# Performance work log

Measured on AMD Instinct MI355X. Metric: run time of the kernel, lower is better.

The kernel has to match this reference:

```python
import jax, jax.numpy as jnp
import numpy as np

INPUT_DIM, HIDDEN, HEADS = 310, 64, 8
WINDOW, PERIOD = 5, 3
NEG_INF = -jnp.inf


def _masks(seq_len):
    i = jnp.arange(seq_len)[:, None]
    j = jnp.arange(seq_len)[None, :]
    local = jnp.abs(i - j) <= WINDOW
    sparse = (j % PERIOD == 0) | (i == j)
    to_add = lambda m: jnp.where(m, 0.0, NEG_INF).astype(jnp.float32)
    return to_add(local), to_add(sparse)


def _mha(xp, in_w, in_b, out_w, out_b, mask):
    # xp: [B,S,E]; in_w: [3E,E]; out_w: [E,E]; mask: [S,S] additive
    B, S, E = xp.shape
    d = E // HEADS
    qkv = xp @ in_w.T + in_b                      # [B,S,3E]
    q, k, v = jnp.split(qkv, 3, axis=-1)
    split_heads = lambda t: t.reshape(B, S, HEADS, d).transpose(0, 2, 1, 3)
    q, k, v = split_heads(q), split_heads(k), split_heads(v)
    scores = jnp.einsum('bhqd,bhkd->bhqk', q, k) / jnp.sqrt(jnp.float32(d))
    scores = scores + mask                         # broadcast [S,S]
    attn = jax.nn.softmax(scores, axis=-1)
    o = jnp.einsum('bhqk,bhkd->bhqd', attn, v)
    o = o.transpose(0, 2, 1, 3).reshape(B, S, E)
    return o @ out_w.T + out_b


def setup_inputs() -> dict:
    key = jax.random.key(0)
    ks = jax.random.split(key, 16)
    E = HIDDEN
    s = lambda fan: 1.0 / np.sqrt(fan)
    u = lambda k, shape, fan: jax.random.uniform(k, shape, jnp.float32, -s(fan), s(fan))
    return {
        'x': jax.random.normal(ks[0], (16, 1024, INPUT_DIM), jnp.float32),
        'proj_w': u(ks[1], (E, INPUT_DIM), INPUT_DIM),
        'proj_b': u(ks[2], (E,), INPUT_DIM),
        'loc_in_w': u(ks[3], (3 * E, E), E),
        'loc_in_b': jnp.zeros((3 * E,), jnp.float32),
        'loc_out_w': u(ks[4], (E, E), E),
        'loc_out_b': jnp.zeros((E,), jnp.float32),
        'glob_in_w': u(ks[5], (3 * E, E), E),
        'glob_in_b': jnp.zeros((3 * E,), jnp.float32),
        'glob_out_w': u(ks[6], (E, E), E),
        'glob_out_b': jnp.zeros((E,), jnp.float32),
        'fusion_w': u(ks[7], (E, 2 * E), 2 * E),
        'fusion_b': u(ks[8], (E,), 2 * E),
        'pool_w1': u(ks[9], (E // 2, E), E),
        'pool_b1': u(ks[10], (E // 2,), E),
        'pool_w2': u(ks[11], (1, E // 2), E // 2),
        'pool_b2': u(ks[12], (1,), E // 2),
    }


def reference(x, proj_w, proj_b, loc_in_w, loc_in_b, loc_out_w, loc_out_b,
              glob_in_w, glob_in_b, glob_out_w, glob_out_b,
              fusion_w, fusion_b, pool_w1, pool_b1, pool_w2, pool_b2):
    B, S, _ = x.shape
    local_mask, sparse_mask = _masks(S)
    xp = x @ proj_w.T + proj_b                     # [B,S,E]
    local_out = _mha(xp, loc_in_w, loc_in_b, loc_out_w, loc_out_b, local_mask)
    global_out = _mha(xp, glob_in_w, glob_in_b, glob_out_w, glob_out_b, sparse_mask)
    fused = jnp.concatenate([local_out, global_out], axis=-1) @ fusion_w.T + fusion_b
    scores = jnp.tanh(fused @ pool_w1.T + pool_b1) @ pool_w2.T + pool_b2  # [B,S,1]
    w = jax.nn.softmax(scores, axis=1)             # softmax over seq dim
    return jnp.sum(fused * w, axis=1)              # [B,E]
```

## Files before the change

### kernel.cpp

```cpp
#include <hip/hip_runtime.h>


typedef __attribute__((ext_vector_type(8))) short short8;
typedef __attribute__((ext_vector_type(4))) float float4v;

#define INV_SQRT8 0.3535533905932738f

__device__ __forceinline__ float4 ld4(const float* p) { return *(const float4*)p; }

__device__ __forceinline__ float4 f4fma(float s, float4 w, float4 a) {
  a.x = fmaf(s, w.x, a.x); a.y = fmaf(s, w.y, a.y);
  a.z = fmaf(s, w.z, a.z); a.w = fmaf(s, w.w, a.w);
  return a;
}

__device__ __forceinline__ void bsplit(float x, short& h, short& l) {
  unsigned xb = __float_as_uint(x);
  unsigned hb = (xb + 0x7fffu + ((xb >> 16) & 1u)) & 0xffff0000u;
  h = (short)(hb >> 16);
  float lf = x - __uint_as_float(hb);
  unsigned lb = __float_as_uint(lf);
  l = (short)((lb + 0x7fffu + ((lb >> 16) & 1u)) >> 16);
}

__global__ __launch_bounds__(256) void prep_w(
    const float* __restrict__ pw, const float* __restrict__ liw,
    const float* __restrict__ giw, const float* __restrict__ fw,
    const float* __restrict__ low, const float* __restrict__ gow,
    const float* __restrict__ lob, const float* __restrict__ gob,
    const float* __restrict__ fb,
    short* __restrict__ wb, float* __restrict__ bc, float* __restrict__ numden)
{
  unsigned idx = blockIdx.x * 256 + threadIdx.x;
  float v; unsigned ho, lo_;
  if (idx < 20480u) {
    unsigned r = idx / 320u, k = idx - r * 320u;
    v = (k < 310u) ? pw[r * 310u + k] : 0.f;
    ho = 0u + idx; lo_ = 20480u + idx;
  } else if (idx < 32768u) {
    unsigned i = idx - 20480u; v = liw[i]; ho = 40960u + i; lo_ = 53248u + i;
  } else if (idx < 45056u) {
    unsigned i = idx - 32768u; v = giw[i]; ho = 65536u + i; lo_ = 77824u + i;
  } else {
    unsigned i = idx - 45056u;
    unsigned n = i >> 7, k = i & 127u;
    float s = 0.f;
    if (k < 64u) {
      for (int e = 0; e < 64; e++) s += fw[n * 128 + e] * low[e * 64 + k];
    } else {
      for (int e = 0; e < 64; e++) s += fw[n * 128 + 64 + e] * gow[e * 64 + (k - 64u)];
    }
    v = s; ho = 90112u + i; lo_ = 98304u + i;
  }
  short h, l; bsplit(v, h, l);
  wb[ho] = h; wb[lo_] = l;
  if (idx < 64u) {
    float b = fb[idx];
    for (int e = 0; e < 64; e++)
      b += lob[e] * fw[idx * 128 + e] + gob[e] * fw[idx * 128 + 64 + e];
    bc[idx] = b;
  }
  if (idx < 1040u) numden[idx] = 0.f;
}

__global__ __launch_bounds__(256) void gemm_proj(
    const float* __restrict__ X,
    const short* __restrict__ Wh, const short* __restrict__ Wl,
    const float* __restrict__ bias,
    short* __restrict__ Ch, short* __restrict__ Cl)
{
  const int lane = threadIdx.x & 63;
  const int w = threadIdx.x >> 6;
  const int q = lane >> 4, r = lane & 15;
  const int m0 = blockIdx.x * 64 + w * 16;
  const int n0 = blockIdx.y * 32;

  float bv0 = bias[n0 + r], bv1 = bias[n0 + 16 + r];
  float4v acc0 = {bv0, bv0, bv0, bv0};
  float4v acc1 = {bv1, bv1, bv1, bv1};

  const float* arow = X + (size_t)(m0 + r) * 310;

  #pragma unroll
  for (int ks = 0; ks < 10; ks++) {
    const int k0 = ks * 32 + q * 8;
    float av[8];
    if (ks < 9) {
      const float* ap = arow + k0;
      #pragma unroll
      for (int t = 0; t < 4; t++) {
        float2 f = *(const float2*)(ap + t * 2);
        av[t*2] = f.x; av[t*2+1] = f.y;
      }
    } else {
      #pragma unroll
      for (int j = 0; j < 8; j++) {
        int kidx = k0 + j;
        av[j] = (kidx < 310) ? arow[kidx] : 0.f;
      }
    }
    short8 ah, al;
    #pragma unroll
    for (int i = 0; i < 8; i++) { short h, l; bsplit(av[i], h, l); ah[i]=h; al[i]=l; }
    short8 bh0 = *(const short8*)(Wh + (size_t)(n0 + r) * 320 + k0);
    short8 bl0 = *(const short8*)(Wl + (size_t)(n0 + r) * 320 + k0);
    short8 bh1 = *(const short8*)(Wh + (size_t)(n0 + 16 + r) * 320 + k0);
    short8 bl1 = *(const short8*)(Wl + (size_t)(n0 + 16 + r) * 320 + k0);
    acc0 = __builtin_amdgcn_mfma_f32_16x16x32_bf16(al, bh0, acc0, 0, 0, 0);
    acc0 = __builtin_amdgcn_mfma_f32_16x16x32_bf16(ah, bl0, acc0, 0, 0, 0);
    acc0 = __builtin_amdgcn_mfma_f32_16x16x32_bf16(ah, bh0, acc0, 0, 0, 0);
    acc1 = __builtin_amdgcn_mfma_f32_16x16x32_bf16(al, bh1, acc1, 0, 0, 0);
    acc1 = __builtin_amdgcn_mfma_f32_16x16x32_bf16(ah, bl1, acc1, 0, 0, 0);
    acc1 = __builtin_amdgcn_mfma_f32_16x16x32_bf16(ah, bh1, acc1, 0, 0, 0);
  }

  #pragma unroll
  for (int e = 0; e < 4; e++) {
    const int row = m0 + q * 4 + e;
    short h, l;
    bsplit(acc0[e], h, l);
    Ch[(size_t)row * 64 + n0 + r] = h; Cl[(size_t)row * 64 + n0 + r] = l;
    bsplit(acc1[e], h, l);
    Ch[(size_t)row * 64 + n0 + 16 + r] = h; Cl[(size_t)row * 64 + n0 + 16 + r] = l;
  }
}

template<int KP>
__global__ __launch_bounds__(256) void gemm_mfma(
    const short* __restrict__ Ah, const short* __restrict__ Al,
    const short* __restrict__ Wh0, const short* __restrict__ Wl0,
    const short* __restrict__ Wh1, const short* __restrict__ Wl1,
    const float* __restrict__ bias0, const float* __restrict__ bias1,
    float* __restrict__ C0, float* __restrict__ C1, int ldc)
{
  const int z = blockIdx.z;
  const short* Wh = z ? Wh1 : Wh0;
  const short* Wl = z ? Wl1 : Wl0;
  const float* bias = z ? bias1 : bias0;
  float* C = z ? C1 : C0;

  const int lane = threadIdx.x & 63;
  const int w = threadIdx.x >> 6;
  const int q = lane >> 4, r = lane & 15;
  const int m0 = blockIdx.x * 64 + w * 16;
  const int n0 = blockIdx.y * 32;

  float bv0 = bias[n0 + r], bv1 = bias[n0 + 16 + r];
  float4v acc0 = {bv0, bv0, bv0, bv0};
  float4v acc1 = {bv1, bv1, bv1, bv1};

  #pragma unroll
  for (int ks = 0; ks < KP / 32; ks++) {
    const int k0 = ks * 32 + q * 8;
    short8 ah = *(const short8*)(Ah + (size_t)(m0 + r) * KP + k0);
    short8 al = *(const short8*)(Al + (size_t)(m0 + r) * KP + k0);
    short8 bh0 = *(const short8*)(Wh + (size_t)(n0 + r) * KP + k0);
    short8 bl0 = *(const short8*)(Wl + (size_t)(n0 + r) * KP + k0);
    short8 bh1 = *(const short8*)(Wh + (size_t)(n0 + 16 + r) * KP + k0);
    short8 bl1 = *(const short8*)(Wl + (size_t)(n0 + 16 + r) * KP + k0);
    acc0 = __builtin_amdgcn_mfma_f32_16x16x32_bf16(al, bh0, acc0, 0, 0, 0);
    acc0 = __builtin_amdgcn_mfma_f32_16x16x32_bf16(ah, bl0, acc0, 0, 0, 0);
    acc0 = __builtin_amdgcn_mfma_f32_16x16x32_bf16(ah, bh0, acc0, 0, 0, 0);
    acc1 = __builtin_amdgcn_mfma_f32_16x16x32_bf16(al, bh1, acc1, 0, 0, 0);
    acc1 = __builtin_amdgcn_mfma_f32_16x16x32_bf16(ah, bl1, acc1, 0, 0, 0);
    acc1 = __builtin_amdgcn_mfma_f32_16x16x32_bf16(ah, bh1, acc1, 0, 0, 0);
  }

  #pragma unroll
  for (int e = 0; e < 4; e++) {
    const int row = m0 + q * 4 + e;
    C[(size_t)row * ldc + n0 + r] = acc0[e];
    C[(size_t)row * ldc + n0 + 16 + r] = acc1[e];
  }
}

__global__ __launch_bounds__(256) void prep_kv_local(
    const float* __restrict__ qkv_g, const float* __restrict__ qkv_l,
    short* __restrict__ KH, short* __restrict__ KL,
    short* __restrict__ VTh, short* __restrict__ VTl,
    float* __restrict__ o_l)
{
  const int u = blockIdx.x;
  if (u < 4224) {
    unsigned idx = (unsigned)u * 256u + threadIdx.x;
    if (idx < 360448u) {
      unsigned bh = idx / 2816u;
      unsigned rem = idx - bh * 2816u;
      unsigned kk = rem >> 3, d = rem & 7u;
      float v = (kk < 342u)
        ? qkv_g[((size_t)((bh >> 3) * 1024 + kk * 3)) * 192 + 64 + (bh & 7u) * 8 + d]
        : 0.f;
      short h, l; bsplit(v, h, l);
      KH[idx] = h; KL[idx] = l;
    } else if (idx < 1081344u) {
      unsigned j = idx - 360448u;
      unsigned bh = j / 5632u;
      unsigned rem = j - bh * 5632u;
      unsigned n = rem / 352u, kk = rem - n * 352u;
      float v;
      if (n < 8u) {
        v = (kk < 342u)
          ? qkv_g[((size_t)((bh >> 3) * 1024 + kk * 3)) * 192 + 128 + (bh & 7u) * 8 + n]
          : 0.f;
      } else {
        v = (n == 8u) ? 1.f : 0.f;
      }
      short h, l; bsplit(v, h, l);
      VTh[j] = h; VTl[j] = l;
    }
  } else {
    int t = (u - 4224) * 256 + threadIdx.x;
    int h = t & 7;
    int i = (t >> 3) & 1023;
    int b = t >> 13;
    const float* base = qkv_l + (size_t)b * 1024 * 192;
    const float* qp = base + (size_t)i * 192 + h * 8;
    float4 q0 = ld4(qp), q1 = ld4(qp + 4);
    float l = 0.f;
    float4 o0 = make_float4(0.f, 0.f, 0.f, 0.f);
    float4 o1 = make_float4(0.f, 0.f, 0.f, 0.f);
    int jlo = i - 5; if (jlo < 0) jlo = 0;
    int jhi = i + 5; if (jhi > 1023) jhi = 1023;
    for (int j = jlo; j <= jhi; j++) {
      const float* kp = base + (size_t)j * 192 + 64 + h * 8;
      float4 k0 = ld4(kp), k1 = ld4(kp + 4);
      float s = q0.x * k0.x + q0.y * k0.y + q0.z * k0.z + q0.w * k0.w
              + q1.x * k1.x + q1.y * k1.y + q1.z * k1.z + q1.w * k1.w;
      float p = __expf(s * INV_SQRT8);
      l += p;
      float4 v0 = ld4(kp + 64), v1 = ld4(kp + 68);
      o0 = f4fma(p, v0, o0);
      o1 = f4fma(p, v1, o1);
    }
    float inv = 1.f / l;
    float* op = o_l + (size_t)(b * 1024 + i) * 64 + h * 8;
    float4 r0, r1;
    r0.x = o0.x * inv; r0.y = o0.y * inv; r0.z = o0.z * inv; r0.w = o0.w * inv;
    r1.x = o1.x * inv; r1.y = o1.y * inv; r1.z = o1.z * inv; r1.w = o1.w * inv;
    *(float4*)op = r0;
    *(float4*)(op + 4) = r1;
  }
}

__global__ __launch_bounds__(256) void mfma_gattn(
    const float* __restrict__ qkv,
    const short* __restrict__ KH, const short* __restrict__ KL,
    const short* __restrict__ VTh, const short* __restrict__ VTl,
    float* __restrict__ o_g, float* __restrict__ pl)
{
  __shared__ short Pbuf[4][2][2][16][32];
  const int b = blockIdx.x, h = blockIdx.y, qt = blockIdx.z;
  const int w = threadIdx.x >> 6, lane = threadIdx.x & 63;
  const int quad = lane >> 4, r = lane & 15;
  const int bh = b * 8 + h;
  const int m0 = qt * 64 + w * 16;

  const short8 z8 = {0,0,0,0,0,0,0,0};
  short8 qh = z8, ql = z8;
  if (quad == 0) {
    const float* qp = qkv + (size_t)(b * 1024 + m0 + r) * 192 + h * 8;
    #pragma unroll
    for (int d = 0; d < 8; d++) { short hh, ll; bsplit(qp[d], hh, ll); qh[d]=hh; ql[d]=ll; }
  }
  const short* kbase  = KH + (size_t)bh * 2816;
  const short* klbase = KL + (size_t)bh * 2816;
  const short* vhbase = VTh + ((size_t)bh * 16 + r) * 352;
  const short* vlbase = VTl + ((size_t)bh * 16 + r) * 352;

  float4v oacc = {0.f, 0.f, 0.f, 0.f};

  for (int kc = 0; kc < 11; kc++) {
    short8 kh0 = z8, kl0 = z8, kh1 = z8, kl1 = z8;
    if (quad == 0) {
      kh0 = *(const short8*)(kbase  + (size_t)(kc * 32 + r) * 8);
      kl0 = *(const short8*)(klbase + (size_t)(kc * 32 + r) * 8);
      kh1 = *(const short8*)(kbase  + (size_t)(kc * 32 + 16 + r) * 8);
      kl1 = *(const short8*)(klbase + (size_t)(kc * 32 + 16 + r) * 8);
    }
    float4v s0 = {0.f,0.f,0.f,0.f}, s1 = {0.f,0.f,0.f,0.f};
    s0 = __builtin_amdgcn_mfma_f32_16x16x32_bf16(qh, kl0, s0, 0, 0, 0);
    s0 = __builtin_amdgcn_mfma_f32_16x16x32_bf16(ql, kh0, s0, 0, 0, 0);
    s0 = __builtin_amdgcn_mfma_f32_16x16x32_bf16(qh, kh0, s0, 0, 0, 0);
    s1 = __builtin_amdgcn_mfma_f32_16x16x32_bf16(qh, kl1, s1, 0, 0, 0);
    s1 = __builtin_amdgcn_mfma_f32_16x16x32_bf16(ql, kh1, s1, 0, 0, 0);
    s1 = __builtin_amdgcn_mfma_f32_16x16x32_bf16(qh, kh1, s1, 0, 0, 0);

    const int par = kc & 1;
    const int key0 = kc * 32 + r, key1 = key0 + 16;
    #pragma unroll
    for (int e = 0; e < 4; e++) {
      float p0 = (key0 < 342) ? __expf(s0[e] * INV_SQRT8) : 0.f;
      float p1 = (key1 < 342) ? __expf(s1[e] * INV_SQRT8) : 0.f;
      short h0, l0, h1, l1; bsplit(p0, h0, l0); bsplit(p1, h1, l1);
      const int qloc = quad * 4 + e;
      Pbuf[w][par][0][qloc][r]      = h0;
      Pbuf[w][par][0][qloc][16 + r] = h1;
      Pbuf[w][par][1][qloc][r]      = l0;
      Pbuf[w][par][1][qloc][16 + r] = l1;
    }
    short8 pA = *(const short8*)&Pbuf[w][par][0][r][quad * 8];
    short8 pB = *(const short8*)&Pbuf[w][par][1][r][quad * 8];
    short8 vh = *(const short8*)(vhbase + kc * 32 + quad * 8);
    short8 vl = *(const short8*)(vlbase + kc * 32 + quad * 8);
    oacc = __builtin_amdgcn_mfma_f32_16x16x32_bf16(pA, vl, oacc, 0, 0, 0);
    oacc = __builtin_amdgcn_mfma_f32_16x16x32_bf16(pB, vh, oacc, 0, 0, 0);
    oacc = __builtin_amdgcn_mfma_f32_16x16x32_bf16(pA, vh, oacc, 0, 0, 0);
  }

  #pragma unroll
  for (int e = 0; e < 4; e++) {
    const int orow = b * 1024 + m0 + quad * 4 + e;
    if (r < 8)       o_g[(size_t)orow * 64 + h * 8 + r] = oacc[e];
    else if (r == 8) pl[(size_t)orow * 8 + h] = oacc[e];
  }
}

__global__ __launch_bounds__(256) void gemm_fuse_score(
    const float* __restrict__ o_l, const float* __restrict__ o_g,
    const float* __restrict__ pl, const float* __restrict__ qkv_g,
    const short* __restrict__ Wh, const short* __restrict__ Wl,
    const float* __restrict__ bc,
    const float* __restrict__ pw1, const float* __restrict__ pb1,
    const float* __restrict__ pw2, const float* __restrict__ pb2,
    float* __restrict__ num, float* __restrict__ den)
{
  __shared__ float Ls[64][68];
  __shared__ float partial[4][64];
  const int tid = threadIdx.x;
  const int lane = tid & 63, w = tid >> 6;
  const int quad = lane >> 4, r = lane & 15;
  const int bx = blockIdx.x;
  const int m0 = bx * 64 + w * 16;

  float4v acc[4];
  #pragma unroll
  for (int g = 0; g < 4; g++) {
    float bv = bc[g * 16 + r];
    float4v t = {bv, bv, bv, bv};
    acc[g] = t;
  }

  #pragma unroll
  for (int ks = 0; ks < 4; ks++) {
    const int k0 = ks * 32 + quad * 8;
    const int row = m0 + r;
    float av[8];
    if (ks < 2) {
      const float* ap = o_l + (size_t)row * 64 + k0;
      float4 f0 = ld4(ap), f1 = ld4(ap + 4);
      av[0]=f0.x; av[1]=f0.y; av[2]=f0.z; av[3]=f0.w;
      av[4]=f1.x; av[5]=f1.y; av[6]=f1.z; av[7]=f1.w;
    } else {
      const int off = k0 - 64;
      const int h = off >> 3;
      const float* op = o_g + (size_t)row * 64 + off;
      float4 O0 = ld4(op), O1 = ld4(op + 4);
      float l = pl[(size_t)row * 8 + h];
      const int i = row & 1023;
      if (i % 3 != 0) {
        const float* base = qkv_g + (size_t)row * 192;
        const float* qp = base + h * 8;
        const float* kpp = base + 64 + h * 8;
        const float* vp = base + 128 + h * 8;
        float4 q0 = ld4(qp), q1 = ld4(qp + 4);
        float4 k0v = ld4(kpp), k1v = ld4(kpp + 4);
        float s = q0.x*k0v.x + q0.y*k0v.y + q0.z*k0v.z + q0.w*k0v.w
                + q1.x*k1v.x + q1.y*k1v.y + q1.z*k1v.z + q1.w*k1v.w;
        float p = __expf(s * INV_SQRT8);
        float4 v0 = ld4(vp), v1 = ld4(vp + 4);
        O0 = f4fma(p, v0, O0); O1 = f4fma(p, v1, O1);
        l += p;
      }
      float inv = 1.f / l;
      av[0]=O0.x*inv; av[1]=O0.y*inv; av[2]=O0.z*inv; av[3]=O0.w*inv;
      av[4]=O1.x*inv; av[5]=O1.y*inv; av[6]=O1.z*inv; av[7]=O1.w*inv;
    }
    short8 ah, al;
    #pragma unroll
    for (int i2 = 0; i2 < 8; i2++) { short h2, l2; bsplit(av[i2], h2, l2); ah[i2]=h2; al[i2]=l2; }
    #pragma unroll
    for (int g = 0; g < 4; g++) {
      short8 bh = *(const short8*)(Wh + (size_t)(g * 16 + r) * 128 + k0);
      short8 bl = *(const short8*)(Wl + (size_t)(g * 16 + r) * 128 + k0);
      acc[g] = __builtin_amdgcn_mfma_f32_16x16x32_bf16(al, bh, acc[g], 0, 0, 0);
      acc[g] = __builtin_amdgcn_mfma_f32_16x16x32_bf16(ah, bl, acc[g], 0, 0, 0);
      acc[g] = __builtin_amdgcn_mfma_f32_16x16x32_bf16(ah, bh, acc[g], 0, 0, 0);
    }
  }

  #pragma unroll
  for (int g = 0; g < 4; g++)
    #pragma unroll
    for (int e = 0; e < 4; e++)
      Ls[w * 16 + quad * 4 + e][g * 16 + r] = acc[g][e];
  __syncthreads();

  float4 fr[16];
  #pragma unroll
  for (int e = 0; e < 16; e++) fr[e] = *(float4*)&Ls[lane][e * 4];

  float psc = 0.f;
  #pragma unroll
  for (int jj = 0; jj < 8; jj++) {
    const int j = w * 8 + jj;
    const float* wr = pw1 + j * 64;
    float hj = pb1[j];
    #pragma unroll
    for (int e = 0; e < 16; e++) {
      float4 wv = ld4(wr + e * 4);
      hj += fr[e].x * wv.x + fr[e].y * wv.y + fr[e].z * wv.z + fr[e].w * wv.w;
    }
    float e2 = __expf(2.f * hj);
    psc += ((e2 - 1.f) / (e2 + 1.f)) * pw2[j];
  }
  partial[w][lane] = psc;
  __syncthreads();
  if (w == 0) {
    const int b = bx >> 4;
    float sc = pb2[0] + partial[0][lane] + partial[1][lane]
             + partial[2][lane] + partial[3][lane];
    float p = __expf(sc);
    #pragma unroll
    for (int e = 0; e < 16; e++) {
      Ls[lane][e*4+0] = p * fr[e].x; Ls[lane][e*4+1] = p * fr[e].y;
      Ls[lane][e*4+2] = p * fr[e].z; Ls[lane][e*4+3] = p * fr[e].w;
    }
    float colsum = 0.f;
    #pragma unroll 8
    for (int s = 0; s < 64; s++) colsum += Ls[s][lane];
    atomicAdd(&num[b * 64 + lane], colsum);
    float ps = p;
    #pragma unroll
    for (int off = 32; off > 0; off >>= 1)
      ps += __shfl_xor(ps, off, 64);
    if (lane == 0) atomicAdd(&den[b], ps);
  }
}

__global__ __launch_bounds__(1024) void finalize(
    const float* __restrict__ num, const float* __restrict__ den,
    float* __restrict__ out)
{
  int t = threadIdx.x;
  out[t] = num[t] / den[t >> 6];
}

extern "C" void kernel_launch(void* const* d_in, const int* in_sizes, int n_in,
                              void* d_out, int out_size, void* d_ws, size_t ws_size,
                              hipStream_t stream)
{
  const float* x          = (const float*)d_in[0];
  const float* proj_w     = (const float*)d_in[1];
  const float* proj_b     = (const float*)d_in[2];
  const float* loc_in_w   = (const float*)d_in[3];
  const float* loc_in_b   = (const float*)d_in[4];
  const float* loc_out_w  = (const float*)d_in[5];
  const float* loc_out_b  = (const float*)d_in[6];
  const float* glob_in_w  = (const float*)d_in[7];
  const float* glob_in_b  = (const float*)d_in[8];
  const float* glob_out_w = (const float*)d_in[9];
  const float* glob_out_b = (const float*)d_in[10];
  const float* fusion_w   = (const float*)d_in[11];
  const float* fusion_b   = (const float*)d_in[12];
  const float* pw1        = (const float*)d_in[13];
  const float* pb1        = (const float*)d_in[14];
  const float* pw2        = (const float*)d_in[15];
  const float* pb2        = (const float*)d_in[16];

  float* ws = (float*)d_ws;
  float* qkv_g = ws;
  short* xph   = (short*)(ws + 3538944);
  short* xpl   = (short*)(ws + 4063232);
  float* qkv_l = ws + 4587520;
  float* o_l   = ws + 7733248;
  float* o_g   = ws + 8781824;
  float* pl    = ws + 9830400;
  short* KH    = (short*)(ws + 9961472);
  short* KL    = (short*)(ws + 10141696);
  short* VTh   = (short*)(ws + 10321920);
  short* VTl   = (short*)(ws + 10682368);
  float* bc    = ws + 11042816;
  float* numden= ws + 11042880;
  float* num   = numden;
  float* den   = numden + 1024;
  short* wb    = (short*)(ws + 11043920);
  short* projh = wb;           short* projl = wb + 20480;
  short* linh  = wb + 40960;   short* linl  = wb + 53248;
  short* ginh  = wb + 65536;   short* ginl  = wb + 77824;
  short* wfh   = wb + 90112;   short* wfl   = wb + 98304;
  float* out   = (float*)d_out;

  dim3 blk(256);
  prep_w<<<208, blk, 0, stream>>>(proj_w, loc_in_w, glob_in_w, fusion_w,
                                  loc_out_w, glob_out_w, loc_out_b, glob_out_b,
                                  fusion_b, wb, bc, numden);
  gemm_proj<<<dim3(256, 2), blk, 0, stream>>>(x, projh, projl, proj_b, xph, xpl);
  gemm_mfma<64><<<dim3(256, 6, 2), blk, 0, stream>>>(
      xph, xpl, linh, linl, ginh, ginl, loc_in_b, glob_in_b,
      qkv_l, qkv_g, 192);
  prep_kv_local<<<4736, blk, 0, stream>>>(qkv_g, qkv_l, KH, KL, VTh, VTl, o_l);
  mfma_gattn<<<dim3(16, 8, 16), blk, 0, stream>>>(qkv_g, KH, KL, VTh, VTl, o_g, pl);
  gemm_fuse_score<<<256, blk, 0, stream>>>(
      o_l, o_g, pl, qkv_g, wfh, wfl, bc, pw1, pb1, pw2, pb2, num, den);
  finalize<<<1, dim3(1024), 0, stream>>>(num, den, out);
}
```

Measured before the change: 191.2 us.

## Fuse projection with QKV GEMM and K/V packing; merge global and local attention

The input projection and both QKV projections now run in one kernel. The projected activations stay in shared memory as bf16 hi/lo pairs instead of going through a global round trip. The same kernel scatters the strided global K and transposed V directly into their packed buffers. The constant padding and ones-row of V is initialised in prep_w, and the global attention and local attention kernels merge into one launch. Together this removes two kernel launches and the xp/qkv re-read passes, at the cost of heavy per-thread register use (24 accumulators) and a grid of only 256 blocks for the fused GEMM.

```diff
diff --git a/kernel.cpp b/kernel.cpp
--- a/kernel.cpp
+++ b/kernel.cpp
@@ -29,58 +29,91 @@
     const float* __restrict__ low, const float* __restrict__ gow,
     const float* __restrict__ lob, const float* __restrict__ gob,
     const float* __restrict__ fb,
-    short* __restrict__ wb, float* __restrict__ bc, float* __restrict__ numden)
+    short* __restrict__ wb, float* __restrict__ bc, float* __restrict__ numden,
+    short* __restrict__ VTh, short* __restrict__ VTl)
 {
   unsigned idx = blockIdx.x * 256 + threadIdx.x;
-  float v; unsigned ho, lo_;
-  if (idx < 20480u) {
-    unsigned r = idx / 320u, k = idx - r * 320u;
-    v = (k < 310u) ? pw[r * 310u + k] : 0.f;
-    ho = 0u + idx; lo_ = 20480u + idx;
-  } else if (idx < 32768u) {
-    unsigned i = idx - 20480u; v = liw[i]; ho = 40960u + i; lo_ = 53248u + i;
-  } else if (idx < 45056u) {
-    unsigned i = idx - 32768u; v = giw[i]; ho = 65536u + i; lo_ = 77824u + i;
+  if (idx < 53248u) {
+    float v; unsigned ho, lo_;
+    if (idx < 20480u) {
+      unsigned r = idx / 320u, k = idx - r * 320u;
+      v = (k < 310u) ? pw[r * 310u + k] : 0.f;
+      ho = 0u + idx; lo_ = 20480u + idx;
+    } else if (idx < 32768u) {
+      unsigned i = idx - 20480u; v = liw[i]; ho = 40960u + i; lo_ = 53248u + i;
+    } else if (idx < 45056u) {
+      unsigned i = idx - 32768u; v = giw[i]; ho = 65536u + i; lo_ = 77824u + i;
+    } else {
+      unsigned i = idx - 45056u;
+      unsigned n = i >> 7, k = i & 127u;
+      float s = 0.f;
+      if (k < 64u) {
+        for (int e = 0; e < 64; e++) s += fw[n * 128 + e] * low[e * 64 + k];
+      } else {
+        for (int e = 0; e < 64; e++) s += fw[n * 128 + 64 + e] * gow[e * 64 + (k - 64u)];
+      }
+      v = s; ho = 90112u + i; lo_ = 98304u + i;
+    }
+    short h, l; bsplit(v, h, l);
+    wb[ho] = h; wb[lo_] = l;
+    if (idx < 64u) {
+      float b = fb[idx];
+      for (int e = 0; e < 64; e++)
+        b += lob[e] * fw[idx * 128 + e] + gob[e] * fw[idx * 128 + 64 + e];
+      bc[idx] = b;
+    }
+    if (idx < 1040u) numden[idx] = 0.f;
   } else {
-    unsigned i = idx - 45056u;
-    unsigned n = i >> 7, k = i & 127u;
-    float s = 0.f;
-    if (k < 64u) {
-      for (int e = 0; e < 64; e++) s += fw[n * 128 + e] * low[e * 64 + k];
-    } else {
-      for (int e = 0; e < 64; e++) s += fw[n * 128 + 64 + e] * gow[e * 64 + (k - 64u)];
-    }
-    v = s; ho = 90112u + i; lo_ = 98304u + i;
-  }
-  short h, l; bsplit(v, h, l);
-  wb[ho] = h; wb[lo_] = l;
-  if (idx < 64u) {
-    float b = fb[idx];
-    for (int e = 0; e < 64; e++)
-      b += lob[e] * fw[idx * 128 + e] + gob[e] * fw[idx * 128 + 64 + e];
-    bc[idx] = b;
-  }
-  if (idx < 1040u) numden[idx] = 0.f;
-}
-
-__global__ __launch_bounds__(256) void gemm_proj(
+    unsigned t = idx - 53248u;
+    if (t < 370688u) {
+      unsigned pos; short hv = 0;
+      if (t < 360448u) {
+        unsigned bh = t / 2816u;
+        unsigned rem = t - bh * 2816u;
+        unsigned n8 = rem / 352u;
+        unsigned kk = rem - n8 * 352u;
+        pos = (bh * 16u + 8u + n8) * 352u + kk;
+        if (n8 == 0u) hv = (short)0x3F80;
+      } else {
+        unsigned t2 = t - 360448u;
+        unsigned bh = t2 / 80u;
+        unsigned rem = t2 - bh * 80u;
+        unsigned n = rem / 10u;
+        unsigned kk = 342u + (rem - n * 10u);
+        pos = (bh * 16u + n) * 352u + kk;
+      }
+      VTh[pos] = hv; VTl[pos] = 0;
+    }
+  }
+}
+
+__global__ __launch_bounds__(256) void gemm_proj_qkv(
     const float* __restrict__ X,
-    const short* __restrict__ Wh, const short* __restrict__ Wl,
-    const float* __restrict__ bias,
-    short* __restrict__ Ch, short* __restrict__ Cl)
+    const short* __restrict__ PWh, const short* __restrict__ PWl,
+    const float* __restrict__ pb,
+    const short* __restrict__ LWh, const short* __restrict__ LWl,
+    const short* __restrict__ GWh, const short* __restrict__ GWl,
+    const float* __restrict__ lb, const float* __restrict__ gb,
+    float* __restrict__ qkv_l, float* __restrict__ qkv_g,
+    short* __restrict__ KH, short* __restrict__ KL,
+    short* __restrict__ VTh, short* __restrict__ VTl)
 {
+  __shared__ __align__(16) short XPH[64][72];
+  __shared__ __align__(16) short XPL[64][72];
   const int lane = threadIdx.x & 63;
   const int w = threadIdx.x >> 6;
   const int q = lane >> 4, r = lane & 15;
-  const int m0 = blockIdx.x * 64 + w * 16;
-  const int n0 = blockIdx.y * 32;
-
-  float bv0 = bias[n0 + r], bv1 = bias[n0 + 16 + r];
-  float4v acc0 = {bv0, bv0, bv0, bv0};
-  float4v acc1 = {bv1, bv1, bv1, bv1};
-
+  const int mloc = w * 16;
+  const int m0 = blockIdx.x * 64 + mloc;
+
+  float4v accp[4];
+  #pragma unroll
+  for (int g = 0; g < 4; g++) {
+    float bv = pb[g * 16 + r];
+    float4v t = {bv, bv, bv, bv};
+    accp[g] = t;
+  }
   const float* arow = X + (size_t)(m0 + r) * 310;
-
   #pragma unroll
   for (int ks = 0; ks < 10; ks++) {
     const int k0 = ks * 32 + q * 8;
@@ -102,114 +135,161 @@
     short8 ah, al;
     #pragma unroll
     for (int i = 0; i < 8; i++) { short h, l; bsplit(av[i], h, l); ah[i]=h; al[i]=l; }
-    short8 bh0 = *(const short8*)(Wh + (size_t)(n0 + r) * 320 + k0);
-    short8 bl0 = *(const short8*)(Wl + (size_t)(n0 + r) * 320 + k0);
-    short8 bh1 = *(const short8*)(Wh + (size_t)(n0 + 16 + r) * 320 + k0);
-    short8 bl1 = *(const short8*)(Wl + (size_t)(n0 + 16 + r) * 320 + k0);
-    acc0 = __builtin_amdgcn_mfma_f32_16x16x32_bf16(al, bh0, acc0, 0, 0, 0);
-    acc0 = __builtin_amdgcn_mfma_f32_16x16x32_bf16(ah, bl0, acc0, 0, 0, 0);
-    acc0 = __builtin_amdgcn_mfma_f32_16x16x32_bf16(ah, bh0, acc0, 0, 0, 0);
-    acc1 = __builtin_amdgcn_mfma_f32_16x16x32_bf16(al, bh1, acc1, 0, 0, 0);
-    acc1 = __builtin_amdgcn_mfma_f32_16x16x32_bf16(ah, bl1, acc1, 0, 0, 0);
-    acc1 = __builtin_amdgcn_mfma_f32_16x16x32_bf16(ah, bh1, acc1, 0, 0, 0);
-  }
-
+    #pragma unroll
+    for (int g = 0; g < 4; g++) {
+      short8 bh = *(const short8*)(PWh + (size_t)(g * 16 + r) * 320 + k0);
+      short8 bl = *(const short8*)(PWl + (size_t)(g * 16 + r) * 320 + k0);
+      accp[g] = __builtin_amdgcn_mfma_f32_16x16x32_bf16(al, bh, accp[g], 0, 0, 0);
+      accp[g] = __builtin_amdgcn_mfma_f32_16x16x32_bf16(ah, bl, accp[g], 0, 0, 0);
+      accp[g] = __builtin_amdgcn_mfma_f32_16x16x32_bf16(ah, bh, accp[g], 0, 0, 0);
+    }
+  }
+  #pragma unroll
+  for (int g = 0; g < 4; g++)
+    #pragma unroll
+    for (int e = 0; e < 4; e++) {
+      short h, l; bsplit(accp[g][e], h, l);
+      XPH[mloc + q * 4 + e][g * 16 + r] = h;
+      XPL[mloc + q * 4 + e][g * 16 + r] = l;
+    }
+
+  float4v acc[2][12];
+  #pragma unroll
+  for (int nf = 0; nf < 12; nf++) {
+    float bv0 = lb[nf * 16 + r], bv1 = gb[nf * 16 + r];
+    float4v t0 = {bv0, bv0, bv0, bv0};
+    float4v t1 = {bv1, bv1, bv1, bv1};
+    acc[0][nf] = t0; acc[1][nf] = t1;
+  }
+  #pragma unroll
+  for (int ks = 0; ks < 2; ks++) {
+    const int k0 = ks * 32 + q * 8;
+    short8 ah = *(const short8*)&XPH[mloc + r][k0];
+    short8 al = *(const short8*)&XPL[mloc + r][k0];
+    #pragma unroll
+    for (int nf = 0; nf < 12; nf++) {
+      short8 bh0 = *(const short8*)(LWh + (size_t)(nf * 16 + r) * 64 + k0);
+      short8 bl0 = *(const short8*)(LWl + (size_t)(nf * 16 + r) * 64 + k0);
+      acc[0][nf] = __builtin_amdgcn_mfma_f32_16x16x32_bf16(al, bh0, acc[0][nf], 0, 0, 0);
+      acc[0][nf] = __builtin_amdgcn_mfma_f32_16x16x32_bf16(ah, bl0, acc[0][nf], 0, 0, 0);
+      acc[0][nf] = __builtin_amdgcn_mfma_f32_16x16x32_bf16(ah, bh0, acc[0][nf], 0, 0, 0);
+      short8 bh1 = *(const short8*)(GWh + (size_t)(nf * 16 + r) * 64 + k0);
+      short8 bl1 = *(const short8*)(GWl + (size_t)(nf * 16 + r) * 64 + k0);
+      acc[1][nf] = __builtin_amdgcn_mfma_f32_16x16x32_bf16(al, bh1, acc[1][nf], 0, 0, 0);
+      acc[1][nf] = __builtin_amdgcn_mfma_f32_16x16x32_bf16(ah, bl1, acc[1][nf], 0, 0, 0);
+      acc[1][nf] = __builtin_amdgcn_mfma_f32_16x16x32_bf16(ah, bh1, acc[1][nf], 0, 0, 0);
+    }
+  }
+
+  const int b = m0 >> 10;
+  const int bh8 = b * 8;
   #pragma unroll
   for (int e = 0; e < 4; e++) {
     const int row = m0 + q * 4 + e;
-    short h, l;
-    bsplit(acc0[e], h, l);
-    Ch[(size_t)row * 64 + n0 + r] = h; Cl[(size_t)row * 64 + n0 + r] = l;
-    bsplit(acc1[e], h, l);
-    Ch[(size_t)row * 64 + n0 + 16 + r] = h; Cl[(size_t)row * 64 + n0 + 16 + r] = l;
-  }
-}
-
-template<int KP>
-__global__ __launch_bounds__(256) void gemm_mfma(
-    const short* __restrict__ Ah, const short* __restrict__ Al,
-    const short* __restrict__ Wh0, const short* __restrict__ Wl0,
-    const short* __restrict__ Wh1, const short* __restrict__ Wl1,
-    const float* __restrict__ bias0, const float* __restrict__ bias1,
-    float* __restrict__ C0, float* __restrict__ C1, int ldc)
+    const int i = row & 1023;
+    #pragma unroll
+    for (int nf = 0; nf < 12; nf++) {
+      qkv_l[(size_t)row * 192 + nf * 16 + r] = acc[0][nf][e];
+      qkv_g[(size_t)row * 192 + nf * 16 + r] = acc[1][nf][e];
+    }
+    if (i % 3 == 0) {
+      const int kk = i / 3;
+      #pragma unroll
+      for (int nf = 4; nf < 12; nf++) {
+        const int col = nf * 16 + r;
+        float v = acc[1][nf][e];
+        short h, l; bsplit(v, h, l);
+        if (col < 128) {
+          const int ck = col - 64;
+          const int hh = ck >> 3, d = ck & 7;
+          KH[(size_t)(bh8 + hh) * 2816 + kk * 8 + d] = h;
+          KL[(size_t)(bh8 + hh) * 2816 + kk * 8 + d] = l;
+        } else {
+          const int cv = col - 128;
+          const int hh = cv >> 3, d = cv & 7;
+          VTh[((size_t)(bh8 + hh) * 16 + d) * 352 + kk] = h;
+          VTl[((size_t)(bh8 + hh) * 16 + d) * 352 + kk] = l;
+        }
+      }
+    }
+  }
+}
+
+__global__ __launch_bounds__(256) void attn(
+    const float* __restrict__ qkv_g, const float* __restrict__ qkv_l,
+    const short* __restrict__ KH, const short* __restrict__ KL,
+    const short* __restrict__ VTh, const short* __restrict__ VTl,
+    float* __restrict__ o_g, float* __restrict__ pl, float* __restrict__ o_l)
 {
-  const int z = blockIdx.z;
-  const short* Wh = z ? Wh1 : Wh0;
-  const short* Wl = z ? Wl1 : Wl0;
-  const float* bias = z ? bias1 : bias0;
-  float* C = z ? C1 : C0;
-
-  const int lane = threadIdx.x & 63;
-  const int w = threadIdx.x >> 6;
-  const int q = lane >> 4, r = lane & 15;
-  const int m0 = blockIdx.x * 64 + w * 16;
-  const int n0 = blockIdx.y * 32;
-
-  float bv0 = bias[n0 + r], bv1 = bias[n0 + 16 + r];
-  float4v acc0 = {bv0, bv0, bv0, bv0};
-  float4v acc1 = {bv1, bv1, bv1, bv1};
-
-  #pragma unroll
-  for (int ks = 0; ks < KP / 32; ks++) {
-    const int k0 = ks * 32 + q * 8;
-    short8 ah = *(const short8*)(Ah + (size_t)(m0 + r) * KP + k0);
-    short8 al = *(const short8*)(Al + (size_t)(m0 + r) * KP + k0);
-    short8 bh0 = *(const short8*)(Wh + (size_t)(n0 + r) * KP + k0);
-    short8 bl0 = *(const short8*)(Wl + (size_t)(n0 + r) * KP + k0);
-    short8 bh1 = *(const short8*)(Wh + (size_t)(n0 + 16 + r) * KP + k0);
-    short8 bl1 = *(const short8*)(Wl + (size_t)(n0 + 16 + r) * KP + k0);
-    acc0 = __builtin_amdgcn_mfma_f32_16x16x32_bf16(al, bh0, acc0, 0, 0, 0);
-    acc0 = __builtin_amdgcn_mfma_f32_16x16x32_bf16(ah, bl0, acc0, 0, 0, 0);
-    acc0 = __builtin_amdgcn_mfma_f32_16x16x32_bf16(ah, bh0, acc0, 0, 0, 0);
-    acc1 = __builtin_amdgcn_mfma_f32_16x16x32_bf16(al, bh1, acc1, 0, 0, 0);
-    acc1 = __builtin_amdgcn_mfma_f32_16x16x32_bf16(ah, bl1, acc1, 0, 0, 0);
-    acc1 = __builtin_amdgcn_mfma_f32_16x16x32_bf16(ah, bh1, acc1, 0, 0, 0);
-  }
-
-  #pragma unroll
-  for (int e = 0; e < 4; e++) {
-    const int row = m0 + q * 4 + e;
-    C[(size_t)row * ldc + n0 + r] = acc0[e];
-    C[(size_t)row * ldc + n0 + 16 + r] = acc1[e];
-  }
-}
-
-__global__ __launch_bounds__(256) void prep_kv_local(
-    const float* __restrict__ qkv_g, const float* __restrict__ qkv_l,
-    short* __restrict__ KH, short* __restrict__ KL,
-    short* __restrict__ VTh, short* __restrict__ VTl,
-    float* __restrict__ o_l)
-{
+  __shared__ short Pbuf[4][2][2][16][32];
   const int u = blockIdx.x;
-  if (u < 4224) {
-    unsigned idx = (unsigned)u * 256u + threadIdx.x;
-    if (idx < 360448u) {
-      unsigned bh = idx / 2816u;
-      unsigned rem = idx - bh * 2816u;
-      unsigned kk = rem >> 3, d = rem & 7u;
-      float v = (kk < 342u)
-        ? qkv_g[((size_t)((bh >> 3) * 1024 + kk * 3)) * 192 + 64 + (bh & 7u) * 8 + d]
-        : 0.f;
-      short h, l; bsplit(v, h, l);
-      KH[idx] = h; KL[idx] = l;
-    } else if (idx < 1081344u) {
-      unsigned j = idx - 360448u;
-      unsigned bh = j / 5632u;
-      unsigned rem = j - bh * 5632u;
-      unsigned n = rem / 352u, kk = rem - n * 352u;
-      float v;
-      if (n < 8u) {
-        v = (kk < 342u)
-          ? qkv_g[((size_t)((bh >> 3) * 1024 + kk * 3)) * 192 + 128 + (bh & 7u) * 8 + n]
-          : 0.f;
-      } else {
-        v = (n == 8u) ? 1.f : 0.f;
-      }
-      short h, l; bsplit(v, h, l);
-      VTh[j] = h; VTl[j] = l;
+  if (u < 2048) {
+    const int qt = u & 15, h = (u >> 4) & 7, b = u >> 7;
+    const int w = threadIdx.x >> 6, lane = threadIdx.x & 63;
+    const int quad = lane >> 4, r = lane & 15;
+    const int bh = b * 8 + h;
+    const int m0 = qt * 64 + w * 16;
+
+    const short8 z8 = {0,0,0,0,0,0,0,0};
+    short8 qh = z8, ql = z8;
+    if (quad == 0) {
+      const float* qp = qkv_g + (size_t)(b * 1024 + m0 + r) * 192 + h * 8;
+      #pragma unroll
+      for (int d = 0; d < 8; d++) { short hh, ll; bsplit(qp[d], hh, ll); qh[d]=hh; ql[d]=ll; }
+    }
+    const short* kbase  = KH + (size_t)bh * 2816;
+    const short* klbase = KL + (size_t)bh * 2816;
+    const short* vhbase = VTh + ((size_t)bh * 16 + r) * 352;
+    const short* vlbase = VTl + ((size_t)bh * 16 + r) * 352;
+
+    float4v oacc = {0.f, 0.f, 0.f, 0.f};
+
+    for (int kc = 0; kc < 11; kc++) {
+      short8 kh0 = z8, kl0 = z8, kh1 = z8, kl1 = z8;
+      if (quad == 0) {
+        kh0 = *(const short8*)(kbase  + (size_t)(kc * 32 + r) * 8);
+        kl0 = *(const short8*)(klbase + (size_t)(kc * 32 + r) * 8);
+        kh1 = *(const short8*)(kbase  + (size_t)(kc * 32 + 16 + r) * 8);
+        kl1 = *(const short8*)(klbase + (size_t)(kc * 32 + 16 + r) * 8);
+      }
+      float4v s0 = {0.f,0.f,0.f,0.f}, s1 = {0.f,0.f,0.f,0.f};
+      s0 = __builtin_amdgcn_mfma_f32_16x16x32_bf16(qh, kl0, s0, 0, 0, 0);
+      s0 = __builtin_amdgcn_mfma_f32_16x16x32_bf16(ql, kh0, s0, 0, 0, 0);
+      s0 = __builtin_amdgcn_mfma_f32_16x16x32_bf16(qh, kh0, s0, 0, 0, 0);
+      s1 = __builtin_amdgcn_mfma_f32_16x16x32_bf16(qh, kl1, s1, 0, 0, 0);
+      s1 = __builtin_amdgcn_mfma_f32_16x16x32_bf16(ql, kh1, s1, 0, 0, 0);
+      s1 = __builtin_amdgcn_mfma_f32_16x16x32_bf16(qh, kh1, s1, 0, 0, 0);
+
+      const int par = kc & 1;
+      const int key0 = kc * 32 + r, key1 = key0 + 16;
+      #pragma unroll
+      for (int e = 0; e < 4; e++) {
+        float p0 = (key0 < 342) ? __expf(s0[e] * INV_SQRT8) : 0.f;
+        float p1 = (key1 < 342) ? __expf(s1[e] * INV_SQRT8) : 0.f;
+        short h0, l0, h1, l1; bsplit(p0, h0, l0); bsplit(p1, h1, l1);
+        const int qloc = quad * 4 + e;
+        Pbuf[w][par][0][qloc][r]      = h0;
+        Pbuf[w][par][0][qloc][16 + r] = h1;
+        Pbuf[w][par][1][qloc][r]      = l0;
+        Pbuf[w][par][1][qloc][16 + r] = l1;
+      }
+      short8 pA = *(const short8*)&Pbuf[w][par][0][r][quad * 8];
+      short8 pB = *(const short8*)&Pbuf[w][par][1][r][quad * 8];
+      short8 vh = *(const short8*)(vhbase + kc * 32 + quad * 8);
+      short8 vl = *(const short8*)(vlbase + kc * 32 + quad * 8);
+      oacc = __builtin_amdgcn_mfma_f32_16x16x32_bf16(pA, vl, oacc, 0, 0, 0);
+      oacc = __builtin_amdgcn_mfma_f32_16x16x32_bf16(pB, vh, oacc, 0, 0, 0);
+      oacc = __builtin_amdgcn_mfma_f32_16x16x32_bf16(pA, vh, oacc, 0, 0, 0);
+    }
+
+    #pragma unroll
+    for (int e = 0; e < 4; e++) {
+      const int orow = b * 1024 + m0 + quad * 4 + e;
+      if (r < 8)       o_g[(size_t)orow * 64 + h * 8 + r] = oacc[e];
+      else if (r == 8) pl[(size_t)orow * 8 + h] = oacc[e];
     }
   } else {
-    int t = (u - 4224) * 256 + threadIdx.x;
+    int t = (u - 2048) * 256 + threadIdx.x;
     int h = t & 7;
     int i = (t >> 3) & 1023;
     int b = t >> 13;
@@ -239,79 +319,6 @@
     r1.x = o1.x * inv; r1.y = o1.y * inv; r1.z = o1.z * inv; r1.w = o1.w * inv;
     *(float4*)op = r0;
     *(float4*)(op + 4) = r1;
-  }
-}
-
-__global__ __launch_bounds__(256) void mfma_gattn(
-    const float* __restrict__ qkv,
-    const short* __restrict__ KH, const short* __restrict__ KL,
-    const short* __restrict__ VTh, const short* __restrict__ VTl,
-    float* __restrict__ o_g, float* __restrict__ pl)
-{
-  __shared__ short Pbuf[4][2][2][16][32];
-  const int b = blockIdx.x, h = blockIdx.y, qt = blockIdx.z;
-  const int w = threadIdx.x >> 6, lane = threadIdx.x & 63;
-  const int quad = lane >> 4, r = lane & 15;
-  const int bh = b * 8 + h;
-  const int m0 = qt * 64 + w * 16;
-
-  const short8 z8 = {0,0,0,0,0,0,0,0};
-  short8 qh = z8, ql = z8;
-  if (quad == 0) {
-    const float* qp = qkv + (size_t)(b * 1024 + m0 + r) * 192 + h * 8;
-    #pragma unroll
-    for (int d = 0; d < 8; d++) { short hh, ll; bsplit(qp[d], hh, ll); qh[d]=hh; ql[d]=ll; }
-  }
-  const short* kbase  = KH + (size_t)bh * 2816;
-  const short* klbase = KL + (size_t)bh * 2816;
-  const short* vhbase = VTh + ((size_t)bh * 16 + r) * 352;
-  const short* vlbase = VTl + ((size_t)bh * 16 + r) * 352;
-
-  float4v oacc = {0.f, 0.f, 0.f, 0.f};
-
-  for (int kc = 0; kc < 11; kc++) {
-    short8 kh0 = z8, kl0 = z8, kh1 = z8, kl1 = z8;
-    if (quad == 0) {
-      kh0 = *(const short8*)(kbase  + (size_t)(kc * 32 + r) * 8);
-      kl0 = *(const short8*)(klbase + (size_t)(kc * 32 + r) * 8);
-      kh1 = *(const short8*)(kbase  + (size_t)(kc * 32 + 16 + r) * 8);
-      kl1 = *(const short8*)(klbase + (size_t)(kc * 32 + 16 + r) * 8);
-    }
-    float4v s0 = {0.f,0.f,0.f,0.f}, s1 = {0.f,0.f,0.f,0.f};
-    s0 = __builtin_amdgcn_mfma_f32_16x16x32_bf16(qh, kl0, s0, 0, 0, 0);
-    s0 = __builtin_amdgcn_mfma_f32_16x16x32_bf16(ql, kh0, s0, 0, 0, 0);
-    s0 = __builtin_amdgcn_mfma_f32_16x16x32_bf16(qh, kh0, s0, 0, 0, 0);
-    s1 = __builtin_amdgcn_mfma_f32_16x16x32_bf16(qh, kl1, s1, 0, 0, 0);
-    s1 = __builtin_amdgcn_mfma_f32_16x16x32_bf16(ql, kh1, s1, 0, 0, 0);
-    s1 = __builtin_amdgcn_mfma_f32_16x16x32_bf16(qh, kh1, s1, 0, 0, 0);
-
-    const int par = kc & 1;
-    const int key0 = kc * 32 + r, key1 = key0 + 16;
-    #pragma unroll
-    for (int e = 0; e < 4; e++) {
-      float p0 = (key0 < 342) ? __expf(s0[e] * INV_SQRT8) : 0.f;
-      float p1 = (key1 < 342) ? __expf(s1[e] * INV_SQRT8) : 0.f;
-      short h0, l0, h1, l1; bsplit(p0, h0, l0); bsplit(p1, h1, l1);
-      const int qloc = quad * 4 + e;
-      Pbuf[w][par][0][qloc][r]      = h0;
-      Pbuf[w][par][0][qloc][16 + r] = h1;
-      Pbuf[w][par][1][qloc][r]      = l0;
-      Pbuf[w][par][1][qloc][16 + r] = l1;
-    }
-    short8 pA = *(const short8*)&Pbuf[w][par][0][r][quad * 8];
-    short8 pB = *(const short8*)&Pbuf[w][par][1][r][quad * 8];
-    short8 vh = *(const short8*)(vhbase + kc * 32 + quad * 8);
-    short8 vl = *(const short8*)(vlbase + kc * 32 + quad * 8);
-    oacc = __builtin_amdgcn_mfma_f32_16x16x32_bf16(pA, vl, oacc, 0, 0, 0);
-    oacc = __builtin_amdgcn_mfma_f32_16x16x32_bf16(pB, vh, oacc, 0, 0, 0);
-    oacc = __builtin_amdgcn_mfma_f32_16x16x32_bf16(pA, vh, oacc, 0, 0, 0);
-  }
-
-  #pragma unroll
-  for (int e = 0; e < 4; e++) {
-    const int orow = b * 1024 + m0 + quad * 4 + e;
-    if (r < 8)       o_g[(size_t)orow * 64 + h * 8 + r] = oacc[e];
-    else if (r == 8) pl[(size_t)orow * 8 + h] = oacc[e];
   }
 }
 
@@ -469,8 +476,6 @@
 
   float* ws = (float*)d_ws;
   float* qkv_g = ws;
-  short* xph   = (short*)(ws + 3538944);
-  short* xpl   = (short*)(ws + 4063232);
   float* qkv_l = ws + 4587520;
   float* o_l   = ws + 7733248;
   float* o_g   = ws + 8781824;
@@ -491,15 +496,13 @@
   float* out   = (float*)d_out;
 
   dim3 blk(256);
-  prep_w<<<208, blk, 0, stream>>>(proj_w, loc_in_w, glob_in_w, fusion_w,
-                                  loc_out_w, glob_out_w, loc_out_b, glob_out_b,
-                                  fusion_b, wb, bc, numden);
-  gemm_proj<<<dim3(256, 2), blk, 0, stream>>>(x, projh, projl, proj_b, xph, xpl);
-  gemm_mfma<64><<<dim3(256, 6, 2), blk, 0, stream>>>(
-      xph, xpl, linh, linl, ginh, ginl, loc_in_b, glob_in_b,
-      qkv_l, qkv_g, 192);
-  prep_kv_local<<<4736, blk, 0, stream>>>(qkv_g, qkv_l, KH, KL, VTh, VTl, o_l);
-  mfma_gattn<<<dim3(16, 8, 16), blk, 0, stream>>>(qkv_g, KH, KL, VTh, VTl, o_g, pl);
+  prep_w<<<1656, blk, 0, stream>>>(proj_w, loc_in_w, glob_in_w, fusion_w,
+                                   loc_out_w, glob_out_w, loc_out_b, glob_out_b,
+                                   fusion_b, wb, bc, numden, VTh, VTl);
+  gemm_proj_qkv<<<256, blk, 0, stream>>>(
+      x, projh, projl, proj_b, linh, linl, ginh, ginl, loc_in_b, glob_in_b,
+      qkv_l, qkv_g, KH, KL, VTh, VTl);
+  attn<<<2560, blk, 0, stream>>>(qkv_g, qkv_l, KH, KL, VTh, VTl, o_g, pl, o_l);
   gemm_fuse_score<<<256, blk, 0, stream>>>(
       o_l, o_g, pl, qkv_g, wfh, wfl, bc, pw1, pb1, pw2, pb2, num, den);
   finalize<<<1, dim3(1024), 0, stream>>>(num, den, out);
```

New measurement: 173.6 us. 9.2% less time.
